# Kernel optimization log

Hardware: AMD Instinct MI355X
Metric: run time of the kernel (lower is better)

## Reference

```python
import jax, jax.numpy as jnp
import numpy as np


def setup_inputs() -> dict:
    key = jax.random.key(0)
    k1, k2, k3, k4 = jax.random.split(key, 4)
    B, S, E = 4, 2048, 2048
    x = jax.random.normal(k1, (B, S, E), dtype=jnp.float32)
    w_query = jax.random.normal(k2, (E, E), dtype=jnp.float32)
    w_key = jax.random.normal(k3, (E, E), dtype=jnp.float32)
    w_value = jax.random.normal(k4, (E, E), dtype=jnp.float32)
    return {"x": x, "w_query": w_query, "w_key": w_key, "w_value": w_value}


def reference(x, w_query, w_key, w_value):
    B, S, E = x.shape
    H = 16
    Dh = E // H  # query_size
    scale = 1.0 / jnp.sqrt(jnp.float32(Dh))
    # NOTE: original uses reshape (NOT transpose) from (B,S,H,Dh) -> (B,H,S,Dh),
    # a pure reinterpretation of the flat buffer. Replicate with direct reshape.
    q = (x @ w_query).reshape(B, H, S, Dh)
    k = (x @ w_key).reshape(B, H, S, Dh)
    v = (x @ w_value).reshape(B, H, S, Dh)
    scores = jnp.einsum("bhqd,bhkd->bhqk", q, k) * scale
    # original applies Softmax(dim=0) to each (S,S) score matrix -> query axis
    soft = jax.nn.softmax(scores, axis=2)
    attn = jnp.einsum("bhqk,bhkd->bhqd", soft, v)  # (B,H,S,Dh)
    # original: reshape (B,H,S,Dh)->(B,S,H,Dh)->(B,S,E), both pure reshapes
    return attn.reshape(B, S, E)
```

## Files before the change

### kernel.cpp

```cpp
#include <hip/hip_runtime.h>
#include <math.h>

typedef _Float16 half_t;
typedef __attribute__((ext_vector_type(8))) _Float16 f16x8;
typedef __attribute__((ext_vector_type(4))) _Float16 f16x4;
typedef __attribute__((ext_vector_type(4))) float f32x4;
typedef __attribute__((ext_vector_type(16))) float f32x16;

#define MFMA __builtin_amdgcn_mfma_f32_16x16x32_f16
#define MFMA32 __builtin_amdgcn_mfma_f32_32x32x16_f16
#define K1C (0.08838834764831845f * 1.4426950408889634f)
#define RLO (1.0f / 2048.0f)

__device__ inline void gld16(const void* g, void* l) {
  __builtin_amdgcn_global_load_lds(
      (const __attribute__((address_space(1))) uint32_t*)g,
      (__attribute__((address_space(3))) uint32_t*)l, 16, 0, 0);
}

__global__ __launch_bounds__(256) void split_x(const float* __restrict__ X,
                                               half_t* __restrict__ Xh,
                                               half_t* __restrict__ Xl) {
  size_t i = (size_t)blockIdx.x * 256 + threadIdx.x;
  const size_t stride = (size_t)gridDim.x * 256;
  for (size_t p = i; p < 4194304; p += stride) {
    f32x4 v = ((const f32x4*)X)[p];
    f16x4 h, l;
#pragma unroll
    for (int j = 0; j < 4; ++j) {
      half_t hh = (half_t)v[j];
      h[j] = hh;
      l[j] = (half_t)((v[j] - (float)hh) * 2048.0f);
    }
    ((f16x4*)Xh)[p] = h;
    ((f16x4*)Xl)[p] = l;
  }
}

__global__ __launch_bounds__(256) void wtrans_split(const float* __restrict__ W,
                                                    half_t* __restrict__ Wh,
                                                    half_t* __restrict__ Wl) {
  __shared__ float T[64][68];
  const int tid = threadIdx.x;
  const int k0 = blockIdx.x * 64, n0 = blockIdx.y * 64;
#pragma unroll
  for (int t = 0; t < 4; ++t) {
    int s = t * 256 + tid;
    int kr = s >> 4, nc = (s & 15) * 4;
    f32x4 v = *(const f32x4*)&W[(size_t)(k0 + kr) * 2048 + n0 + nc];
#pragma unroll
    for (int j = 0; j < 4; ++j) T[nc + j][kr] = v[j];
  }
  __syncthreads();
#pragma unroll
  for (int t = 0; t < 4; ++t) {
    int s = t * 256 + tid;
    int nr = s >> 4, kc = (s & 15) * 4;
    f16x4 h, l;
#pragma unroll
    for (int j = 0; j < 4; ++j) {
      float q = T[nr][kc + j];
      half_t hh = (half_t)q;
      h[j] = hh;
      l[j] = (half_t)((q - (float)hh) * 2048.0f);
    }
    *(f16x4*)&Wh[(size_t)(n0 + nr) * 2048 + k0 + kc] = h;
    *(f16x4*)&Wl[(size_t)(n0 + nr) * 2048 + k0 + kc] = l;
  }
}

#define STAGE_P(nb, kn) do {                                                  \
    _Pragma("unroll")                                                         \
    for (int t_ = 0; t_ < 2; ++t_) {                                          \
      int s_ = t_ * 256 + tid;                                                \
      int row_ = s_ >> 2;                                                     \
      int lch_ = (s_ & 3) ^ ((row_ >> 1) & 3);       \
      size_t ga_ = (size_t)(m0 + row_) * 2048 + (kn) + lch_ * 8;              \
      size_t gb_ = (size_t)(n0 + row_) * 2048 + (kn) + lch_ * 8;              \
      gld16(&Xh[ga_], &sm[nb][s_ * 8]);                                       \
      gld16(&Wh[gb_], &sm[nb][4096 + s_ * 8]);                                \
      if constexpr (MODE == 0) {                                              \
        gld16(&Xl[ga_], &sm[nb][8192 + s_ * 8]);                              \
        gld16(&Wl[gb_], &sm[nb][12288 + s_ * 8]);                             \
      }                                                                       \
    }                                                                         \
  } while (0)

template <int MODE>
__global__ __launch_bounds__(256, MODE == 0 ? 2 : 4) void proj_mfma(
    const half_t* __restrict__ Xh, const half_t* __restrict__ Xl,
    const half_t* __restrict__ Wh, const half_t* __restrict__ Wl,
    half_t* __restrict__ Ch, half_t* __restrict__ Cl) {
  __shared__ half_t sm[2][MODE == 0 ? 16384 : 8192];
  const int tid = threadIdx.x;
  const int lid = blockIdx.x;
  const int swz = (lid & 7) * 128 + (lid >> 3);
  const int m0 = (swz >> 4) << 7, n0 = (swz & 15) << 7;
  const int w = tid >> 6, lane = tid & 63, r5 = lane & 31, hi = lane >> 5;
  const int wr = w >> 1, wc = w & 1;
  const int rsw = (r5 >> 1) & 3;
  f32x16 acc0[2][2], accX[2][2];
#pragma unroll
  for (int i = 0; i < 2; ++i)
#pragma unroll
    for (int j = 0; j < 2; ++j) {
#pragma unroll
      for (int r = 0; r < 16; ++r) { acc0[i][j][r] = 0.f; accX[i][j][r] = 0.f; }
    }
  STAGE_P(0, 0);
  __syncthreads();
  for (int k0 = 0; k0 < 2048; k0 += 32) {
    const int buf = (k0 >> 5) & 1;
    if (k0 < 2016) STAGE_P(buf ^ 1, k0 + 32);
#pragma unroll
    for (int ks = 0; ks < 2; ++ks) {
      const int ch = ((ks << 1) | hi) ^ rsw;
      f16x8 a0[2], a1[2], b0[2], b1[2];
#pragma unroll
      for (int i = 0; i < 2; ++i) {
        int ar = wr * 64 + i * 32 + r5;
        int br = wc * 64 + i * 32 + r5;
        a0[i] = *(const f16x8*)&sm[buf][ar * 32 + ch * 8];
        b0[i] = *(const f16x8*)&sm[buf][4096 + br * 32 + ch * 8];
        if constexpr (MODE == 0) {
          a1[i] = *(const f16x8*)&sm[buf][8192 + ar * 32 + ch * 8];
          b1[i] = *(const f16x8*)&sm[buf][12288 + br * 32 + ch * 8];
        }
      }
#pragma unroll
      for (int i = 0; i < 2; ++i)
#pragma unroll
        for (int j = 0; j < 2; ++j) {
          acc0[i][j] = MFMA32(a0[i], b0[j], acc0[i][j], 0, 0, 0);
          if constexpr (MODE == 0) {
            accX[i][j] = MFMA32(a0[i], b1[j], accX[i][j], 0, 0, 0);
            accX[i][j] = MFMA32(a1[i], b0[j], accX[i][j], 0, 0, 0);
          }
        }
    }
    __syncthreads();
  }
#pragma unroll
  for (int i = 0; i < 2; ++i)
#pragma unroll
    for (int j = 0; j < 2; ++j) {
      int mb = m0 + wr * 64 + i * 32 + 4 * hi;
      int n = n0 + wc * 64 + j * 32 + r5;
#pragma unroll
      for (int r = 0; r < 16; ++r) {
        int mrow = mb + (r & 3) + 8 * (r >> 2);
        float q;
        if constexpr (MODE == 0) q = acc0[i][j][r] + accX[i][j][r] * RLO;
        else q = acc0[i][j][r];
        half_t hh = (half_t)q;
        size_t o = (size_t)mrow * 2048 + n;
        Ch[o] = hh;
        if constexpr (MODE == 0) Cl[o] = (half_t)((q - (float)hh) * 2048.0f);
      }
    }
}

__global__ __launch_bounds__(256) void transpose_v(const half_t* __restrict__ V,
                                                   half_t* __restrict__ Vt) {
  __shared__ half_t T[128 * 128];
  const int tid = threadIdx.x;
  const int bh = blockIdx.y, k0 = blockIdx.x * 128;
  const size_t base = (size_t)bh << 18;
#pragma unroll
  for (int t = 0; t < 8; ++t) {
    int s = t * 256 + tid;
    int kr = s >> 4, ch = s & 15;
    int pc = ch ^ ((kr >> 3) & 15);
    *(f16x8*)&T[kr * 128 + pc * 8] =
        *(const f16x8*)&V[base + (size_t)(k0 + kr) * 128 + ch * 8];
  }
  __syncthreads();
#pragma unroll
  for (int t = 0; t < 8; ++t) {
    int s = t * 256 + tid;
    int d = s >> 4, kc = s & 15;
    f16x8 o;
#pragma unroll
    for (int j = 0; j < 8; ++j) {
      int kr = kc * 8 + j;
      int pc = (d >> 3) ^ (kc & 15);
      o[j] = T[kr * 128 + pc * 8 + (d & 7)];
    }
    *(f16x8*)&Vt[base + (size_t)d * 2048 + k0 + kc * 8] = o;
  }
}

#define STAGE_Q(nb, qn) do {                                                  \
    int r0_ = tid >> 4, cl0_ = tid & 15;                                      \
    size_t o0_ = base + (size_t)((qn) + r0_) * 128 + ((cl0_ ^ r0_) << 3);     \
    gld16(&Qh[o0_], &sQ0[nb][tid << 3]);                                      \
    gld16(&Ql[o0_], &sQ1[nb][tid << 3]);                                      \
    int r1_ = 16 + r0_;                                                       \
    size_t o1_ = base + (size_t)((qn) + r1_) * 128 + ((cl0_ ^ (r1_ & 15)) << 3); \
    gld16(&Qh[o1_], &sQ0[nb][(256 + tid) << 3]);                              \
    gld16(&Ql[o1_], &sQ1[nb][(256 + tid) << 3]);                              \
  } while (0)

__global__ __launch_bounds__(256, 2) void stats_mfma(
    const half_t* __restrict__ Qh, const half_t* __restrict__ Ql,
    const half_t* __restrict__ Kh, const half_t* __restrict__ Kl,
    float* __restrict__ Mp, float* __restrict__ Zp) {
  __shared__ half_t sQ0[2][4096], sQ1[2][4096];
  const int tid = threadIdx.x;
  const int w = tid >> 6, lane = tid & 63, c = lane & 15, g = lane >> 4;
  const int lid = blockIdx.y * 8 + blockIdx.x;
  const int bh = (lid & 7) * 8 + ((lid >> 3) & 7);
  const int xb = lid >> 6;
  const int qstart = blockIdx.z << 9;
  const size_t base = (size_t)bh << 18;
  const int kb = xb * 256 + w * 64;
  f32x4 z4 = {0.f, 0.f, 0.f, 0.f};
  f16x8 ka0[4][4], ka1[4][4];
#pragma unroll
  for (int kt = 0; kt < 4; ++kt)
#pragma unroll
    for (int ds = 0; ds < 4; ++ds) {
      size_t a = base + (size_t)(kb + kt * 16 + c) * 128 + ds * 32 + g * 8;
      ka0[kt][ds] = *(const f16x8*)&Kh[a];
      ka1[kt][ds] = *(const f16x8*)&Kl[a];
    }
  float m[4][4], z[4][4];
#pragma unroll
  for (int kt = 0; kt < 4; ++kt)
#pragma unroll
    for (int r = 0; r < 4; ++r) { m[kt][r] = -INFINITY; z[kt][r] = 0.f; }
  STAGE_Q(0, qstart);
  __syncthreads();
  for (int t = 0; t < 16; ++t) {
    const int buf = t & 1;
    if (t < 15) STAGE_Q(buf ^ 1, qstart + ((t + 1) << 5));
#pragma unroll
    for (int qh = 0; qh < 2; ++qh) {
      f16x8 q0v[4], q1v[4];
#pragma unroll
      for (int ds = 0; ds < 4; ++ds) {
        int off = ((qh << 4) | c) * 128 + ((((ds << 2) | g) ^ c) << 3);
        q0v[ds] = *(const f16x8*)&sQ0[buf][off];
        q1v[ds] = *(const f16x8*)&sQ1[buf][off];
      }
#pragma unroll
      for (int kt = 0; kt < 4; ++kt) {
        f32x4 A0 = z4, AX = z4;
#pragma unroll
        for (int ds = 0; ds < 4; ++ds) {
          A0 = MFMA(ka0[kt][ds], q0v[ds], A0, 0, 0, 0);
          AX = MFMA(ka0[kt][ds], q1v[ds], AX, 0, 0, 0);
          AX = MFMA(ka1[kt][ds], q0v[ds], AX, 0, 0, 0);
        }
#pragma unroll
        for (int r = 0; r < 4; ++r) {
          float tt = (A0[r] + AX[r] * RLO) * K1C;
          float mo = m[kt][r];
          float mn = fmaxf(mo, tt);
          float e = __builtin_amdgcn_exp2f(fminf(mo, tt) - mn);
          z[kt][r] = (tt <= mo) ? (z[kt][r] + e) : (z[kt][r] * e + 1.0f);
          m[kt][r] = mn;
        }
      }
    }
    __syncthreads();
  }
#pragma unroll
  for (int mask = 1; mask < 16; mask <<= 1)
#pragma unroll
    for (int kt = 0; kt < 4; ++kt)
#pragma unroll
      for (int r = 0; r < 4; ++r) {
        float mo = __shfl_xor(m[kt][r], mask, 64);
        float zo = __shfl_xor(z[kt][r], mask, 64);
        float mn = fmaxf(m[kt][r], mo);
        z[kt][r] = z[kt][r] * __builtin_amdgcn_exp2f(m[kt][r] - mn) +
                   zo * __builtin_amdgcn_exp2f(mo - mn);
        m[kt][r] = mn;
      }
  if (c == 0) {
    const int pb = (blockIdx.z << 17) + (bh << 11);
#pragma unroll
    for (int kt = 0; kt < 4; ++kt)
#pragma unroll
      for (int r = 0; r < 4; ++r) {
        int idx = pb + kb + kt * 16 + (g << 2) + r;
        Mp[idx] = m[kt][r];
        Zp[idx] = z[kt][r];
      }
  }
}

__global__ __launch_bounds__(256) void stats_finalize(const float* __restrict__ Mp,
                                                      const float* __restrict__ Zp,
                                                      float* __restrict__ C2) {
  int i = blockIdx.x * 256 + threadIdx.x;
  float m = Mp[i], z = Zp[i];
#pragma unroll
  for (int s = 1; s < 4; ++s) {
    float ms = Mp[(s << 17) + i], zs = Zp[(s << 17) + i];
    float mn = fmaxf(m, ms);
    z = z * __builtin_amdgcn_exp2f(m - mn) + zs * __builtin_amdgcn_exp2f(ms - mn);
    m = mn;
  }
  C2[i] = m + __builtin_amdgcn_logf(z);
}

#define STAGE_ATTN(nb, ktn) do {                                              \
    int r_ = tid >> 4, chl_ = tid & 15;                                       \
    size_t ro_ = base + (size_t)((ktn) + r_) * 128 + ((chl_ ^ (r_ & 15)) << 3); \
    gld16(&Kh[ro_], &sKh[nb][tid << 3]);                                      \
    gld16(&Kl[ro_], &sKl[nb][tid << 3]);                                      \
    int d_ = tid >> 2, cvl_ = tid & 3;                                        \
    gld16(&Vt[base + (size_t)d_ * 2048 + (ktn) + ((cvl_ ^ ((d_ >> 1) & 3)) << 3)], \
          &sVs[nb][tid << 3]);                                                \
  } while (0)

__global__ __launch_bounds__(512, 4) void attn_mfma(
    const half_t* __restrict__ Qh, const half_t* __restrict__ Ql,
    const half_t* __restrict__ Kh, const half_t* __restrict__ Kl,
    const half_t* __restrict__ Vt, const float* __restrict__ C2,
    float* __restrict__ O) {
  __shared__ half_t sKh[2][4096], sKl[2][4096], sVs[2][4096];
  __shared__ half_t sP[8][16][40];
  __shared__ float sC2[2048];
  const int tid = threadIdx.x;
  const int w = tid >> 6, lane = tid & 63, c = lane & 15, g = lane >> 4;
  const int lid = blockIdx.y * 16 + blockIdx.x;
  const int bh = (lid & 7) * 8 + ((lid >> 3) & 7);
  const int qx = lid >> 6;
  const size_t base = (size_t)bh << 18;
  const int qb = qx * 128 + w * 16;
  f32x4 z4 = {0.f, 0.f, 0.f, 0.f};
  f16x8 qf0[4], qf1[4];
#pragma unroll
  for (int ds = 0; ds < 4; ++ds) {
    size_t a = base + (size_t)(qb + c) * 128 + ds * 32 + g * 8;
    qf0[ds] = *(const f16x8*)&Qh[a];
    qf1[ds] = *(const f16x8*)&Ql[a];
  }
  f32x4 Oacc[8];
#pragma unroll
  for (int dt = 0; dt < 8; ++dt) Oacc[dt] = z4;
  ((f32x4*)sC2)[tid] = ((const f32x4*)(C2 + ((size_t)bh << 11)))[tid];
  STAGE_ATTN(0, 0);
  __syncthreads();
  for (int t = 0; t < 64; ++t) {
    const int buf = t & 1;
    const int kt = t << 5;
    if (t < 63) STAGE_ATTN(buf ^ 1, kt + 32);
#pragma unroll
    for (int h = 0; h < 2; ++h) {
      f32x4 A0 = z4, AX = z4;
#pragma unroll
      for (int ds = 0; ds < 4; ++ds) {
        int off = ((h << 4) | c) * 128 + ((((ds << 2) | g) ^ c) << 3);
        f16x8 k0v = *(const f16x8*)&sKh[buf][off];
        f16x8 k1v = *(const f16x8*)&sKl[buf][off];
        A0 = MFMA(k0v, qf0[ds], A0, 0, 0, 0);
        AX = MFMA(k0v, qf1[ds], AX, 0, 0, 0);
        AX = MFMA(k1v, qf0[ds], AX, 0, 0, 0);
      }
      f32x4 c2v = *(const f32x4*)&sC2[kt + (h << 4) + (g << 2)];
      f16x4 pv;
#pragma unroll
      for (int r = 0; r < 4; ++r)
        pv[r] = (half_t)__builtin_amdgcn_exp2f((A0[r] + AX[r] * RLO) * K1C - c2v[r]);
      *(f16x4*)&sP[w][c][(h << 4) + (g << 2)] = pv;
    }
    f16x8 pa = *(const f16x8*)&sP[w][c][g << 3];
#pragma unroll
    for (int dt = 0; dt < 8; ++dt) {
      int dd = (dt << 4) + c;
      f16x8 vb = *(const f16x8*)&sVs[buf][dd * 32 + ((g ^ ((dd >> 1) & 3)) << 3)];
      Oacc[dt] = MFMA(pa, vb, Oacc[dt], 0, 0, 0);
    }
    __syncthreads();
  }
#pragma unroll
  for (int dt = 0; dt < 8; ++dt)
#pragma unroll
    for (int r = 0; r < 4; ++r)
      O[base + (size_t)(qb + (g << 2) + r) * 128 + (dt << 4) + c] = Oacc[dt][r];
}

extern "C" void kernel_launch(void* const* d_in, const int* in_sizes, int n_in,
                              void* d_out, int out_size, void* d_ws, size_t ws_size,
                              hipStream_t stream) {
  (void)in_sizes; (void)n_in; (void)out_size; (void)ws_size;
  const float* x = (const float*)d_in[0];
  const float* wq = (const float*)d_in[1];
  const float* wk = (const float*)d_in[2];
  const float* wv = (const float*)d_in[3];
  float* out = (float*)d_out;
  char* ws = (char*)d_ws;
  const size_t S2 = 33554432;
  half_t* Wth = (half_t*)ws;
  half_t* Wtl = (half_t*)(ws + 8388608);
  half_t* Qh = (half_t*)(ws + 16777216);
  half_t* Ql = (half_t*)(ws + 16777216 + S2);
  half_t* Kh = (half_t*)(ws + 16777216 + 2 * S2);
  half_t* Kl = (half_t*)(ws + 16777216 + 3 * S2);
  half_t* Vh = (half_t*)(ws + 16777216 + 4 * S2);
  half_t* Vth = (half_t*)(ws + 16777216 + 5 * S2);
  float* C2 = (float*)(ws + 16777216 + 6 * S2);
  float* Mp = C2 + 131072;
  float* Zp = Mp + 524288;
  half_t* Xh = (half_t*)d_out;
  half_t* Xl = (half_t*)((char*)d_out + S2);
  dim3 b(256);
  split_x<<<2048, b, 0, stream>>>(x, Xh, Xl);
  wtrans_split<<<dim3(32, 32), b, 0, stream>>>(wq, Wth, Wtl);
  proj_mfma<0><<<dim3(1024), b, 0, stream>>>(Xh, Xl, Wth, Wtl, Qh, Ql);
  wtrans_split<<<dim3(32, 32), b, 0, stream>>>(wk, Wth, Wtl);
  proj_mfma<0><<<dim3(1024), b, 0, stream>>>(Xh, Xl, Wth, Wtl, Kh, Kl);
  wtrans_split<<<dim3(32, 32), b, 0, stream>>>(wv, Wth, Wtl);
  proj_mfma<1><<<dim3(1024), b, 0, stream>>>(Xh, Xl, Wth, Wtl, Vh, nullptr);
  transpose_v<<<dim3(16, 64), b, 0, stream>>>(Vh, Vth);
  stats_mfma<<<dim3(8, 64, 4), b, 0, stream>>>(Qh, Ql, Kh, Kl, Mp, Zp);
  stats_finalize<<<dim3(512), b, 0, stream>>>(Mp, Zp, C2);
  attn_mfma<<<dim3(16, 64), dim3(512), 0, stream>>>(Qh, Ql, Kh, Kl, Vth, C2, out);
}
```

Measured before the change: 1.076 ms.

## Switch attention kernel to 32x32 MFMA tiles with 32 query rows per wave

Rewrites the attention pass to use 32x32x16 MFMA instead of 16x16x32. Each wave now owns 32 query rows, so a block covers 256 queries and the grid is halved. The goal is to reuse each staged K/V tile across twice as many queries, cutting LDS and global traffic per unit of work. The P staging buffer moves to a swizzled layout, and the exp argument becomes fused FMAs. Launch bounds drop to one block per CU-occupancy hint, which raises register use (f32x16 accumulators) and lowers occupancy.

```diff
diff --git a/kernel.cpp b/kernel.cpp
--- a/kernel.cpp
+++ b/kernel.cpp
@@ -11,6 +11,7 @@
 #define MFMA32 __builtin_amdgcn_mfma_f32_32x32x16_f16
 #define K1C (0.08838834764831845f * 1.4426950408889634f)
 #define RLO (1.0f / 2048.0f)
+#define K1CR (K1C * RLO)
 
 __device__ inline void gld16(const void* g, void* l) {
   __builtin_amdgcn_global_load_lds(
@@ -316,32 +317,34 @@
           &sVs[nb][tid << 3]);                                                \
   } while (0)
 
-__global__ __launch_bounds__(512, 4) void attn_mfma(
+__global__ __launch_bounds__(512, 1) void attn_mfma(
     const half_t* __restrict__ Qh, const half_t* __restrict__ Ql,
     const half_t* __restrict__ Kh, const half_t* __restrict__ Kl,
     const half_t* __restrict__ Vt, const float* __restrict__ C2,
     float* __restrict__ O) {
   __shared__ half_t sKh[2][4096], sKl[2][4096], sVs[2][4096];
-  __shared__ half_t sP[8][16][40];
+  __shared__ half_t sP[8][1024];
   __shared__ float sC2[2048];
   const int tid = threadIdx.x;
-  const int w = tid >> 6, lane = tid & 63, c = lane & 15, g = lane >> 4;
-  const int lid = blockIdx.y * 16 + blockIdx.x;
+  const int w = tid >> 6, lane = tid & 63, q5 = lane & 31, h = lane >> 5;
+  const int lid = blockIdx.y * 8 + blockIdx.x;
   const int bh = (lid & 7) * 8 + ((lid >> 3) & 7);
   const int qx = lid >> 6;
   const size_t base = (size_t)bh << 18;
-  const int qb = qx * 128 + w * 16;
-  f32x4 z4 = {0.f, 0.f, 0.f, 0.f};
-  f16x8 qf0[4], qf1[4];
-#pragma unroll
-  for (int ds = 0; ds < 4; ++ds) {
-    size_t a = base + (size_t)(qb + c) * 128 + ds * 32 + g * 8;
-    qf0[ds] = *(const f16x8*)&Qh[a];
-    qf1[ds] = *(const f16x8*)&Ql[a];
-  }
-  f32x4 Oacc[8];
-#pragma unroll
-  for (int dt = 0; dt < 8; ++dt) Oacc[dt] = z4;
+  const int qb = qx * 256 + w * 32;
+  const int psw = (q5 >> 1) & 3;
+  f16x8 qfh[8], qfl[8];
+#pragma unroll
+  for (int ds = 0; ds < 8; ++ds) {
+    size_t a = base + (size_t)(qb + q5) * 128 + ds * 16 + h * 8;
+    qfh[ds] = *(const f16x8*)&Qh[a];
+    qfl[ds] = *(const f16x8*)&Ql[a];
+  }
+  f32x16 Oacc[4];
+#pragma unroll
+  for (int dt = 0; dt < 4; ++dt)
+#pragma unroll
+    for (int r = 0; r < 16; ++r) Oacc[dt][r] = 0.f;
   ((f32x4*)sC2)[tid] = ((const f32x4*)(C2 + ((size_t)bh << 11)))[tid];
   STAGE_ATTN(0, 0);
   __syncthreads();
@@ -349,39 +352,51 @@
     const int buf = t & 1;
     const int kt = t << 5;
     if (t < 63) STAGE_ATTN(buf ^ 1, kt + 32);
-#pragma unroll
-    for (int h = 0; h < 2; ++h) {
-      f32x4 A0 = z4, AX = z4;
-#pragma unroll
-      for (int ds = 0; ds < 4; ++ds) {
-        int off = ((h << 4) | c) * 128 + ((((ds << 2) | g) ^ c) << 3);
-        f16x8 k0v = *(const f16x8*)&sKh[buf][off];
-        f16x8 k1v = *(const f16x8*)&sKl[buf][off];
-        A0 = MFMA(k0v, qf0[ds], A0, 0, 0, 0);
-        AX = MFMA(k0v, qf1[ds], AX, 0, 0, 0);
-        AX = MFMA(k1v, qf0[ds], AX, 0, 0, 0);
-      }
-      f32x4 c2v = *(const f32x4*)&sC2[kt + (h << 4) + (g << 2)];
+    f32x16 A0, AX;
+#pragma unroll
+    for (int r = 0; r < 16; ++r) { A0[r] = 0.f; AX[r] = 0.f; }
+#pragma unroll
+    for (int ds = 0; ds < 8; ++ds) {
+      int pc = (ds * 2 + h) ^ (q5 & 15);
+      f16x8 k0v = *(const f16x8*)&sKh[buf][q5 * 128 + pc * 8];
+      f16x8 k1v = *(const f16x8*)&sKl[buf][q5 * 128 + pc * 8];
+      A0 = MFMA32(k0v, qfh[ds], A0, 0, 0, 0);
+      AX = MFMA32(k0v, qfl[ds], AX, 0, 0, 0);
+      AX = MFMA32(k1v, qfh[ds], AX, 0, 0, 0);
+    }
+#pragma unroll
+    for (int rr = 0; rr < 4; ++rr) {
       f16x4 pv;
 #pragma unroll
-      for (int r = 0; r < 4; ++r)
-        pv[r] = (half_t)__builtin_amdgcn_exp2f((A0[r] + AX[r] * RLO) * K1C - c2v[r]);
-      *(f16x4*)&sP[w][c][(h << 4) + (g << 2)] = pv;
-    }
-    f16x8 pa = *(const f16x8*)&sP[w][c][g << 3];
-#pragma unroll
-    for (int dt = 0; dt < 8; ++dt) {
-      int dd = (dt << 4) + c;
-      f16x8 vb = *(const f16x8*)&sVs[buf][dd * 32 + ((g ^ ((dd >> 1) & 3)) << 3)];
-      Oacc[dt] = MFMA(pa, vb, Oacc[dt], 0, 0, 0);
+      for (int j = 0; j < 4; ++j) {
+        int r = rr * 4 + j;
+        float c2 = sC2[kt + j + 8 * rr + 4 * h];
+        float tt = fmaf(AX[r], K1CR, fmaf(A0[r], K1C, -c2));
+        pv[j] = (half_t)__builtin_amdgcn_exp2f(tt);
+      }
+      *(f16x4*)&sP[w][q5 * 32 + ((rr ^ psw) << 3) + h * 4] = pv;
+    }
+#pragma unroll
+    for (int c16 = 0; c16 < 2; ++c16) {
+      int rrp = c16 * 2 + h;
+      f16x8 pa = *(const f16x8*)&sP[w][q5 * 32 + ((rrp ^ psw) << 3)];
+#pragma unroll
+      for (int dt = 0; dt < 4; ++dt) {
+        int d = dt * 32 + q5;
+        int pcv = (c16 * 2 + h) ^ ((q5 >> 1) & 3);
+        f16x8 vb = *(const f16x8*)&sVs[buf][d * 32 + pcv * 8];
+        Oacc[dt] = MFMA32(pa, vb, Oacc[dt], 0, 0, 0);
+      }
     }
     __syncthreads();
   }
 #pragma unroll
-  for (int dt = 0; dt < 8; ++dt)
-#pragma unroll
-    for (int r = 0; r < 4; ++r)
-      O[base + (size_t)(qb + (g << 2) + r) * 128 + (dt << 4) + c] = Oacc[dt][r];
+  for (int dt = 0; dt < 4; ++dt)
+#pragma unroll
+    for (int r = 0; r < 16; ++r) {
+      int qrow = qb + (r & 3) + 8 * (r >> 2) + 4 * h;
+      O[base + (size_t)qrow * 128 + dt * 32 + q5] = Oacc[dt][r];
+    }
 }
 
 extern "C" void kernel_launch(void* const* d_in, const int* in_sizes, int n_in,
@@ -419,5 +434,5 @@
   transpose_v<<<dim3(16, 64), b, 0, stream>>>(Vh, Vth);
   stats_mfma<<<dim3(8, 64, 4), b, 0, stream>>>(Qh, Ql, Kh, Kl, Mp, Zp);
   stats_finalize<<<dim3(512), b, 0, stream>>>(Mp, Zp, C2);
-  attn_mfma<<<dim3(16, 64), dim3(512), 0, stream>>>(Qh, Ql, Kh, Kl, Vth, C2, out);
-}
+  attn_mfma<<<dim3(8, 64), dim3(512), 0, stream>>>(Qh, Ql, Kh, Kl, Vth, C2, out);
+}
```

Measured after the change: 1.108 ms. 3.0% more time.

## Process two query tiles per wave in attention kernel to reuse K/V loads

Applied to the files above, without the earlier changes.

Each wave in the attention kernel now handles 32 query rows (two 16-row tiles) instead of 16, so each block covers 256 queries and the grid is halved. Every K and V fragment loaded from shared memory feeds twice as many MFMAs, and each block streams the full K/V sequence into LDS for twice as many queries. This roughly halves the global and LDS traffic for K/V per output. The cost is about twice the register use for accumulators and Q fragments; the occupancy hint drops to 2 blocks per CU and the grid has fewer blocks.

```diff
diff --git a/kernel.cpp b/kernel.cpp
--- a/kernel.cpp
+++ b/kernel.cpp
@@ -316,32 +316,36 @@
           &sVs[nb][tid << 3]);                                                \
   } while (0)
 
-__global__ __launch_bounds__(512, 4) void attn_mfma(
+__global__ __launch_bounds__(512, 2) void attn_mfma(
     const half_t* __restrict__ Qh, const half_t* __restrict__ Ql,
     const half_t* __restrict__ Kh, const half_t* __restrict__ Kl,
     const half_t* __restrict__ Vt, const float* __restrict__ C2,
     float* __restrict__ O) {
   __shared__ half_t sKh[2][4096], sKl[2][4096], sVs[2][4096];
-  __shared__ half_t sP[8][16][40];
+  __shared__ half_t sP[8][2][16][40];
   __shared__ float sC2[2048];
   const int tid = threadIdx.x;
   const int w = tid >> 6, lane = tid & 63, c = lane & 15, g = lane >> 4;
-  const int lid = blockIdx.y * 16 + blockIdx.x;
+  const int lid = blockIdx.y * 8 + blockIdx.x;
   const int bh = (lid & 7) * 8 + ((lid >> 3) & 7);
   const int qx = lid >> 6;
   const size_t base = (size_t)bh << 18;
-  const int qb = qx * 128 + w * 16;
+  const int qb = qx * 256 + w * 32;
   f32x4 z4 = {0.f, 0.f, 0.f, 0.f};
-  f16x8 qf0[4], qf1[4];
-#pragma unroll
-  for (int ds = 0; ds < 4; ++ds) {
-    size_t a = base + (size_t)(qb + c) * 128 + ds * 32 + g * 8;
-    qf0[ds] = *(const f16x8*)&Qh[a];
-    qf1[ds] = *(const f16x8*)&Ql[a];
-  }
-  f32x4 Oacc[8];
-#pragma unroll
-  for (int dt = 0; dt < 8; ++dt) Oacc[dt] = z4;
+  f16x8 qf0[2][4], qf1[2][4];
+#pragma unroll
+  for (int qq = 0; qq < 2; ++qq)
+#pragma unroll
+    for (int ds = 0; ds < 4; ++ds) {
+      size_t a = base + (size_t)(qb + qq * 16 + c) * 128 + ds * 32 + g * 8;
+      qf0[qq][ds] = *(const f16x8*)&Qh[a];
+      qf1[qq][ds] = *(const f16x8*)&Ql[a];
+    }
+  f32x4 Oacc[2][8];
+#pragma unroll
+  for (int qq = 0; qq < 2; ++qq)
+#pragma unroll
+    for (int dt = 0; dt < 8; ++dt) Oacc[qq][dt] = z4;
   ((f32x4*)sC2)[tid] = ((const f32x4*)(C2 + ((size_t)bh << 11)))[tid];
   STAGE_ATTN(0, 0);
   __syncthreads();
@@ -351,37 +355,49 @@
     if (t < 63) STAGE_ATTN(buf ^ 1, kt + 32);
 #pragma unroll
     for (int h = 0; h < 2; ++h) {
-      f32x4 A0 = z4, AX = z4;
+      f32x4 A0[2] = {z4, z4}, AX[2] = {z4, z4};
 #pragma unroll
       for (int ds = 0; ds < 4; ++ds) {
         int off = ((h << 4) | c) * 128 + ((((ds << 2) | g) ^ c) << 3);
         f16x8 k0v = *(const f16x8*)&sKh[buf][off];
         f16x8 k1v = *(const f16x8*)&sKl[buf][off];
-        A0 = MFMA(k0v, qf0[ds], A0, 0, 0, 0);
-        AX = MFMA(k0v, qf1[ds], AX, 0, 0, 0);
-        AX = MFMA(k1v, qf0[ds], AX, 0, 0, 0);
+#pragma unroll
+        for (int qq = 0; qq < 2; ++qq) {
+          A0[qq] = MFMA(k0v, qf0[qq][ds], A0[qq], 0, 0, 0);
+          AX[qq] = MFMA(k0v, qf1[qq][ds], AX[qq], 0, 0, 0);
+          AX[qq] = MFMA(k1v, qf0[qq][ds], AX[qq], 0, 0, 0);
+        }
       }
       f32x4 c2v = *(const f32x4*)&sC2[kt + (h << 4) + (g << 2)];
-      f16x4 pv;
-#pragma unroll
-      for (int r = 0; r < 4; ++r)
-        pv[r] = (half_t)__builtin_amdgcn_exp2f((A0[r] + AX[r] * RLO) * K1C - c2v[r]);
-      *(f16x4*)&sP[w][c][(h << 4) + (g << 2)] = pv;
-    }
-    f16x8 pa = *(const f16x8*)&sP[w][c][g << 3];
+#pragma unroll
+      for (int qq = 0; qq < 2; ++qq) {
+        f16x4 pv;
+#pragma unroll
+        for (int r = 0; r < 4; ++r)
+          pv[r] = (half_t)__builtin_amdgcn_exp2f(
+              (A0[qq][r] + AX[qq][r] * RLO) * K1C - c2v[r]);
+        *(f16x4*)&sP[w][qq][c][(h << 4) + (g << 2)] = pv;
+      }
+    }
+    f16x8 pa0 = *(const f16x8*)&sP[w][0][c][g << 3];
+    f16x8 pa1 = *(const f16x8*)&sP[w][1][c][g << 3];
 #pragma unroll
     for (int dt = 0; dt < 8; ++dt) {
       int dd = (dt << 4) + c;
       f16x8 vb = *(const f16x8*)&sVs[buf][dd * 32 + ((g ^ ((dd >> 1) & 3)) << 3)];
-      Oacc[dt] = MFMA(pa, vb, Oacc[dt], 0, 0, 0);
+      Oacc[0][dt] = MFMA(pa0, vb, Oacc[0][dt], 0, 0, 0);
+      Oacc[1][dt] = MFMA(pa1, vb, Oacc[1][dt], 0, 0, 0);
     }
     __syncthreads();
   }
 #pragma unroll
-  for (int dt = 0; dt < 8; ++dt)
-#pragma unroll
-    for (int r = 0; r < 4; ++r)
-      O[base + (size_t)(qb + (g << 2) + r) * 128 + (dt << 4) + c] = Oacc[dt][r];
+  for (int qq = 0; qq < 2; ++qq)
+#pragma unroll
+    for (int dt = 0; dt < 8; ++dt)
+#pragma unroll
+      for (int r = 0; r < 4; ++r)
+        O[base + (size_t)(qb + qq * 16 + (g << 2) + r) * 128 + (dt << 4) + c] =
+            Oacc[qq][dt][r];
 }
 
 extern "C" void kernel_launch(void* const* d_in, const int* in_sizes, int n_in,
@@ -419,5 +435,5 @@
   transpose_v<<<dim3(16, 64), b, 0, stream>>>(Vh, Vth);
   stats_mfma<<<dim3(8, 64, 4), b, 0, stream>>>(Qh, Ql, Kh, Kl, Mp, Zp);
   stats_finalize<<<dim3(512), b, 0, stream>>>(Mp, Zp, C2);
-  attn_mfma<<<dim3(16, 64), dim3(512), 0, stream>>>(Qh, Ql, Kh, Kl, Vth, C2, out);
-}
+  attn_mfma<<<dim3(8, 64), dim3(512), 0, stream>>>(Qh, Ql, Kh, Kl, Vth, C2, out);
+}
```

New measurement: 1.094 ms. About the same (+1.7%).
